# Kernel tuning notes

Measured on AMD Instinct MI355X. Metric: run time of the kernel, lower is better.

## Reference

```python
import jax, jax.numpy as jnp
import numpy as np

ITERATIONS = 10
EPS = 1e-8
ALPHA = 1.0
BETA = 1.0


def _conv3x3x3(x):
    # all-ones 3x3x3 kernel, padding=1 (SAME), single channel; NCDHW layout
    k = jnp.ones((1, 1, 3, 3, 3), x.dtype)
    return jax.lax.conv_general_dilated(
        x, k, window_strides=(1, 1, 1), padding='SAME',
        dimension_numbers=('NCDHW', 'OIDHW', 'NCDHW'))


def _soft_skeletonize(x):
    x = jax.nn.sigmoid(x)
    skeleton = x
    for _ in range(ITERATIONS):
        eroded = (_conv3x3x3(skeleton) > 0).astype(x.dtype)
        opened = (_conv3x3x3(eroded) > 0).astype(x.dtype)
        skeleton = jnp.clip(skeleton - opened, 0.0, 1.0)
    return skeleton


def _count_components(binary):
    neighbors = _conv3x3x3(binary)
    mask = binary > 0
    cnt = jnp.sum(mask).astype(binary.dtype)
    # torch.mean(neighbors[mask] + eps) == sum((neighbors+eps)*mask)/cnt
    mean_nb = jnp.sum(jnp.where(mask, neighbors + EPS, 0.0)) / jnp.maximum(cnt, 1.0)
    return (cnt / mean_nb)[None]


def setup_inputs() -> dict:
    key = jax.random.key(0)
    k1, k2 = jax.random.split(key)
    pred = jax.random.normal(k1, (2, 1, 192, 192, 192), dtype=jnp.float32)
    target = jax.random.uniform(k2, (2, 1, 192, 192, 192), dtype=jnp.float32)
    return {"pred": pred, "target": target}


def reference(pred, target):
    pred_prob = jax.nn.sigmoid(pred)
    # NOTE: module applies sigmoid again inside _soft_skeletonize (faithful)
    pred_skeleton = _soft_skeletonize(pred_prob)
    target_skeleton = _soft_skeletonize(target)

    intersection = jnp.sum(pred_skeleton * target_skeleton)
    union = jnp.sum(pred_skeleton) + jnp.sum(target_skeleton)
    skeleton_loss = 1.0 - (2.0 * intersection + EPS) / (union + EPS)

    pred_binary = (pred_prob > 0.5).astype(pred.dtype)
    target_binary = target  # .float() no-op
    pred_components = _count_components(pred_binary)
    target_components = _count_components(target_binary)
    connectivity_loss = jnp.mean(jnp.abs(pred_components - target_components))

    return ALPHA * skeleton_loss + BETA * connectivity_loss
```

## Files before the change

### kernel.cpp

```cpp
#include <hip/hip_runtime.h>
#include <math.h>

#define NN 192
#define PLANE (NN * NN)
#define VOLSZ (NN * NN * NN)
#define ZC 24
#define SLABR 8
#define NSLAB (NN / SLABR)
#define SLOTF (10 * NN)
#define NBIN 8
#define EPSF 1e-8f

template <int MODE>
__device__ __forceinline__ float bval(float u) {
  return (MODE == 0) ? ((u > 0.f) ? 1.f : 0.f) : u;
}

struct PlaneR {
  float4 a, b, c, d;
};

template <int MODE>
__device__ __forceinline__ void consume2(const PlaneR& P, float mA, float mD, float mz,
                                         int lane, float4& sY, float4& sZ,
                                         float4& cY, float4& cZ) {
  const float a0 = bval<MODE>(P.a.x), a1 = bval<MODE>(P.a.y), a2 = bval<MODE>(P.a.z), a3 = bval<MODE>(P.a.w);
  const float b0 = bval<MODE>(P.b.x), b1 = bval<MODE>(P.b.y), b2 = bval<MODE>(P.b.z), b3 = bval<MODE>(P.b.w);
  const float c0 = bval<MODE>(P.c.x), c1 = bval<MODE>(P.c.y), c2 = bval<MODE>(P.c.z), c3 = bval<MODE>(P.c.w);
  const float d0 = bval<MODE>(P.d.x), d1 = bval<MODE>(P.d.y), d2 = bval<MODE>(P.d.z), d3 = bval<MODE>(P.d.w);
  const float u0 = b0 + c0, u1 = b1 + c1, u2 = b2 + c2, u3 = b3 + c3;
  const float tY0 = fmaf(a0, mA, u0), tY1 = fmaf(a1, mA, u1), tY2 = fmaf(a2, mA, u2), tY3 = fmaf(a3, mA, u3);
  const float tZ0 = fmaf(d0, mD, u0), tZ1 = fmaf(d1, mD, u1), tZ2 = fmaf(d2, mD, u2), tZ3 = fmaf(d3, mD, u3);
  const float upY = __shfl_up(tY3, 1), dnY = __shfl_down(tY0, 1);
  const float upZ = __shfl_up(tZ3, 1), dnZ = __shfl_down(tZ0, 1);
  const float tlY = (lane == 0) ? 0.f : upY;
  const float trY = (lane >= 47) ? 0.f : dnY;
  const float tlZ = (lane == 0) ? 0.f : upZ;
  const float trZ = (lane >= 47) ? 0.f : dnZ;
  const float pY01 = tY0 + tY1, pY23 = tY2 + tY3;
  const float pZ01 = tZ0 + tZ1, pZ23 = tZ2 + tZ3;
  sY.x = (tlY + pY01) * mz; sY.y = (pY01 + tY2) * mz; sY.z = (tY1 + pY23) * mz; sY.w = (pY23 + trY) * mz;
  sZ.x = (tlZ + pZ01) * mz; sZ.y = (pZ01 + tZ2) * mz; sZ.z = (tZ1 + pZ23) * mz; sZ.w = (pZ23 + trZ) * mz;
  cY.x = b0; cY.y = b1; cY.z = b2; cY.w = b3;
  cZ.x = c0; cZ.y = c1; cZ.z = c2; cZ.w = c3;
}

#define ACC1(C, SP, SC, SN)                                   \
  {                                                           \
    float m = ((C) > 0.f) ? act : 0.f;                        \
    cnt += m;                                                 \
    acc = fmaf(m, ((SP) + (SC)) + (SN), acc);                 \
  }

#define ACCUM8(snY, snZ)                      \
  ACC1(cY.x, spY.x, scY.x, (snY).x)           \
  ACC1(cY.y, spY.y, scY.y, (snY).y)           \
  ACC1(cY.z, spY.z, scY.z, (snY).z)           \
  ACC1(cY.w, spY.w, scY.w, (snY).w)           \
  ACC1(cZ.x, spZ.x, scZ.x, (snZ).x)           \
  ACC1(cZ.y, spZ.y, scZ.y, (snZ).y)           \
  ACC1(cZ.z, spZ.z, scZ.z, (snZ).z)           \
  ACC1(cZ.w, spZ.w, scZ.w, (snZ).w)

__device__ __forceinline__ void ldsReadP(const float* pl, int slotF, int rbaseF, int xoff, PlaneR& P) {
  const float* p = pl + slotF + rbaseF;
  P.a = *(const float4*)(p + 0 * NN + xoff);
  P.b = *(const float4*)(p + 1 * NN + xoff);
  P.c = *(const float4*)(p + 2 * NN + xoff);
  P.d = *(const float4*)(p + 3 * NN + xoff);
}

__device__ __forceinline__ void stageIssue(const float* __restrict__ base, int z, int gRow0,
                                           int tid, int nQ, float4& g0, float4& g1) {
  const int zz = min(max(z, 0), NN - 1);
  const float* gp = base + (size_t)zz * PLANE + gRow0 * NN;
  g0 = *(const float4*)(gp + 4 * tid);
  if (tid + 256 < nQ) g1 = *(const float4*)(gp + 4 * (tid + 256));
}

__device__ __forceinline__ void stageWrite(float* pl, int slotF, int shiftF, int tid, int nQ,
                                           const float4& g0, const float4& g1) {
  float* q = pl + slotF + shiftF;
  *(float4*)(q + 4 * tid) = g0;
  if (tid + 256 < nQ) *(float4*)(q + 4 * (tid + 256)) = g1;
}

#define STEPX(RS, WS, DO_A, DO_B, ZLD, G0, G1, MZ)                         \
  {                                                                        \
    __syncthreads();                                                       \
    if (DO_A) stageWrite(pl, (WS) * SLOTF, shiftF, tid, nQ, G0, G1);       \
    if (DO_B) stageIssue(base, (ZLD), gRow0, tid, nQ, G0, G1);             \
    PlaneR P;                                                              \
    ldsReadP(pl, (RS) * SLOTF, rbaseF, xoff, P);                           \
    float4 snY, snZ, cnY, cnZ;                                             \
    consume2<MODE>(P, mA, mD, (MZ), lane, snY, snZ, cnY, cnZ);             \
    ACCUM8(snY, snZ);                                                      \
    spY = scY; scY = snY; spZ = scZ; scZ = snZ; cY = cnY; cZ = cnZ;        \
  }

template <int MODE>
__device__ __forceinline__ void sweep(const float* __restrict__ base, int y0, int z0,
                                      float* pl, int tid, float& cnt, float& acc) {
  const int lane = tid & 63;
  const int w = tid >> 6;
  const int xoff = 4 * min(lane, 47);
  const float act = (lane < 48) ? 1.f : 0.f;

  const bool loEdge = (y0 == 0), hiEdge = (y0 + SLABR == NN);
  const int gRow0 = loEdge ? 0 : y0 - 1;
  const int nR = 10 - (loEdge ? 1 : 0) - (hiEdge ? 1 : 0);
  const int nQ = nR * 48;
  const int shiftF = loEdge ? NN : 0;

  const int rbaseF = (2 * w) * NN;
  const float mA = (y0 + 2 * w > 0) ? 1.f : 0.f;
  const float mD = (y0 + 2 * w + 2 < NN) ? 1.f : 0.f;
  const float mzLo = (z0 > 0) ? 1.f : 0.f;
  const float mzHi = (z0 + ZC < NN) ? 1.f : 0.f;

  if (loEdge && tid < 48) {
    const float4 z4 = make_float4(0.f, 0.f, 0.f, 0.f);
#pragma unroll
    for (int r = 0; r < 4; ++r) *(float4*)(pl + r * SLOTF + 4 * tid) = z4;
  }
  if (hiEdge && tid < 48) {
    const float4 z4 = make_float4(0.f, 0.f, 0.f, 0.f);
#pragma unroll
    for (int r = 0; r < 4; ++r) *(float4*)(pl + r * SLOTF + 9 * NN + 4 * tid) = z4;
  }

  float4 a0, a1, b0, b1, c0, c1, gP0, gP1, gQ0, gQ1;
  stageIssue(base, z0 - 1, gRow0, tid, nQ, a0, a1);
  stageIssue(base, z0,     gRow0, tid, nQ, b0, b1);
  stageIssue(base, z0 + 1, gRow0, tid, nQ, c0, c1);
  stageIssue(base, z0 + 2, gRow0, tid, nQ, gP0, gP1);
  stageIssue(base, z0 + 3, gRow0, tid, nQ, gQ0, gQ1);
  stageWrite(pl, 0 * SLOTF, shiftF, tid, nQ, a0, a1);
  stageWrite(pl, 1 * SLOTF, shiftF, tid, nQ, b0, b1);
  stageWrite(pl, 2 * SLOTF, shiftF, tid, nQ, c0, c1);
  __syncthreads();

  float4 spY, scY, spZ, scZ, cY, cZ;
  {
    PlaneR P; float4 j1, j2;
    ldsReadP(pl, 0, rbaseF, xoff, P);
    consume2<MODE>(P, mA, mD, mzLo, lane, spY, spZ, j1, j2);
    ldsReadP(pl, SLOTF, rbaseF, xoff, P);
    consume2<MODE>(P, mA, mD, 1.f, lane, scY, scZ, cY, cZ);
  }

#pragma unroll 1
  for (int j = 0; j < 20; j += 4) {
    STEPX(2, 3, true, true, z0 + 4 + j + 0, gP0, gP1, 1.f);
    STEPX(3, 0, true, true, z0 + 4 + j + 1, gQ0, gQ1, 1.f);
    STEPX(0, 1, true, true, z0 + 4 + j + 2, gP0, gP1, 1.f);
    STEPX(1, 2, true, true, z0 + 4 + j + 3, gQ0, gQ1, 1.f);
  }
  STEPX(2, 3, true, true,  z0 + 24, gP0, gP1, 1.f);
  STEPX(3, 0, true, false, 0,       gQ0, gQ1, 1.f);
  STEPX(0, 1, true, false, 0,       gP0, gP1, 1.f);
  STEPX(1, 2, false, false, 0,      gQ0, gQ1, mzHi);
}

__global__ void init_ws(float* __restrict__ ws) {
  if (threadIdx.x < NBIN * 16) ws[threadIdx.x] = 0.f;
}

__global__ __launch_bounds__(256, 1) void skel_main(const float* __restrict__ pred,
                                                    const float* __restrict__ target,
                                                    float* __restrict__ ws) {
  __shared__ float pl[4 * SLOTF];
  const int b = blockIdx.x;
  const int xcd = b & 7;
  const int s = b >> 3;
  const int vol = s / NSLAB;
  const int slab = s % NSLAB;
  const int z0 = xcd * ZC;
  const int y0 = slab * SLABR;
  const float* base = (vol < 2 ? pred : target) + (size_t)(vol & 1) * VOLSZ;
  const int tid = threadIdx.x;

  float cnt = 0.f, acc = 0.f;
  if (vol < 2) sweep<0>(base, y0, z0, pl, tid, cnt, acc);
  else         sweep<1>(base, y0, z0, pl, tid, cnt, acc);

#pragma unroll
  for (int o = 32; o > 0; o >>= 1) {
    cnt += __shfl_down(cnt, o);
    acc += __shfl_down(acc, o);
  }
  __syncthreads();
  if ((tid & 63) == 0) { pl[tid >> 6] = cnt; pl[4 + (tid >> 6)] = acc; }
  __syncthreads();
  if (tid == 0) {
    const int off = (vol < 2) ? 0 : 2;
    float* sp = &ws[((slab & (NBIN - 1)) << 4) + off];
    atomicAdd(sp + 0, pl[0] + pl[1] + pl[2] + pl[3]);
    atomicAdd(sp + 1, pl[4] + pl[5] + pl[6] + pl[7]);
  }
}

__global__ void finalize(const float* __restrict__ ws, float* __restrict__ out) {
  if (threadIdx.x == 0 && blockIdx.x == 0) {
    float cp = 0.f, ap = 0.f, ct = 0.f, at = 0.f;
#pragma unroll
    for (int i = 0; i < NBIN; ++i) {
      cp += ws[i * 16 + 0];
      ap += ws[i * 16 + 1];
      ct += ws[i * 16 + 2];
      at += ws[i * 16 + 3];
    }
    float mp = (ap + EPSF * cp) / fmaxf(cp, 1.f);
    float Pc = cp / mp;
    float mt = (at + EPSF * ct) / fmaxf(ct, 1.f);
    float Tc = ct / mt;
    out[0] = fabsf(Pc - Tc);
  }
}

extern "C" void kernel_launch(void* const* d_in, const int* in_sizes, int n_in,
                              void* d_out, int out_size, void* d_ws, size_t ws_size,
                              hipStream_t stream) {
  const float* pred = (const float*)d_in[0];
  const float* target = (const float*)d_in[1];
  float* ws = (float*)d_ws;
  float* out = (float*)d_out;

  init_ws<<<1, 128, 0, stream>>>(ws);
  skel_main<<<dim3(768), dim3(256), 0, stream>>>(pred, target, ws);
  finalize<<<1, 64, 0, stream>>>(ws, out);
}
```

Measured before the change: 133.9 us.

## Halve z-chunk depth, double grid, shrink LDS ring to three slots, lighter barrier

Each block now sweeps 12 z-planes instead of 24, so the grid doubles to 1536 blocks, and the z0 mapping still keeps both halves of a z range on the same XCD. The LDS plane ring drops from four slots to three and the step loop is fully unrolled. __syncthreads is replaced by an explicit lgkmcnt wait plus s_barrier with sched barriers, so the barrier does not wait on outstanding global loads. The aim is more parallelism and occupancy; in exchange the z-halo loads are amortized over fewer planes, and the three-slot ring relies on the barrier ordering to avoid overwriting a plane still being read.

Measured after the change: 162.5 us. +21.3%, slower.

```diff
diff --git a/kernel.cpp b/kernel.cpp
--- a/kernel.cpp
+++ b/kernel.cpp
@@ -4,10 +4,11 @@
 #define NN 192
 #define PLANE (NN * NN)
 #define VOLSZ (NN * NN * NN)
-#define ZC 24
+#define ZC 12
 #define SLABR 8
 #define NSLAB (NN / SLABR)
 #define SLOTF (10 * NN)
+#define NSLOT 3
 #define NBIN 8
 #define EPSF 1e-8f
 
@@ -15,6 +16,12 @@
 __device__ __forceinline__ float bval(float u) {
   return (MODE == 0) ? ((u > 0.f) ? 1.f : 0.f) : u;
 }
+
+#define WGB()                                            \
+  asm volatile("s_waitcnt lgkmcnt(0)" ::: "memory");     \
+  __builtin_amdgcn_sched_barrier(0);                     \
+  __builtin_amdgcn_s_barrier();                          \
+  __builtin_amdgcn_sched_barrier(0);
 
 struct PlaneR {
   float4 a, b, c, d;
@@ -87,7 +94,7 @@
 
 #define STEPX(RS, WS, DO_A, DO_B, ZLD, G0, G1, MZ)                         \
   {                                                                        \
-    __syncthreads();                                                       \
+    WGB();                                                                 \
     if (DO_A) stageWrite(pl, (WS) * SLOTF, shiftF, tid, nQ, G0, G1);       \
     if (DO_B) stageIssue(base, (ZLD), gRow0, tid, nQ, G0, G1);             \
     PlaneR P;                                                              \
@@ -121,12 +128,12 @@
   if (loEdge && tid < 48) {
     const float4 z4 = make_float4(0.f, 0.f, 0.f, 0.f);
 #pragma unroll
-    for (int r = 0; r < 4; ++r) *(float4*)(pl + r * SLOTF + 4 * tid) = z4;
+    for (int r = 0; r < NSLOT; ++r) *(float4*)(pl + r * SLOTF + 4 * tid) = z4;
   }
   if (hiEdge && tid < 48) {
     const float4 z4 = make_float4(0.f, 0.f, 0.f, 0.f);
 #pragma unroll
-    for (int r = 0; r < 4; ++r) *(float4*)(pl + r * SLOTF + 9 * NN + 4 * tid) = z4;
+    for (int r = 0; r < NSLOT; ++r) *(float4*)(pl + r * SLOTF + 9 * NN + 4 * tid) = z4;
   }
 
   float4 a0, a1, b0, b1, c0, c1, gP0, gP1, gQ0, gQ1;
@@ -143,23 +150,24 @@
   float4 spY, scY, spZ, scZ, cY, cZ;
   {
     PlaneR P; float4 j1, j2;
-    ldsReadP(pl, 0, rbaseF, xoff, P);
+    ldsReadP(pl, 0 * SLOTF, rbaseF, xoff, P);
     consume2<MODE>(P, mA, mD, mzLo, lane, spY, spZ, j1, j2);
-    ldsReadP(pl, SLOTF, rbaseF, xoff, P);
+    ldsReadP(pl, 1 * SLOTF, rbaseF, xoff, P);
     consume2<MODE>(P, mA, mD, 1.f, lane, scY, scZ, cY, cZ);
   }
 
-#pragma unroll 1
-  for (int j = 0; j < 20; j += 4) {
-    STEPX(2, 3, true, true, z0 + 4 + j + 0, gP0, gP1, 1.f);
-    STEPX(3, 0, true, true, z0 + 4 + j + 1, gQ0, gQ1, 1.f);
-    STEPX(0, 1, true, true, z0 + 4 + j + 2, gP0, gP1, 1.f);
-    STEPX(1, 2, true, true, z0 + 4 + j + 3, gQ0, gQ1, 1.f);
-  }
-  STEPX(2, 3, true, true,  z0 + 24, gP0, gP1, 1.f);
-  STEPX(3, 0, true, false, 0,       gQ0, gQ1, 1.f);
+  STEPX(2, 0, true, true,  z0 + 4,  gP0, gP1, 1.f);
+  STEPX(0, 1, true, true,  z0 + 5,  gQ0, gQ1, 1.f);
+  STEPX(1, 2, true, true,  z0 + 6,  gP0, gP1, 1.f);
+  STEPX(2, 0, true, true,  z0 + 7,  gQ0, gQ1, 1.f);
+  STEPX(0, 1, true, true,  z0 + 8,  gP0, gP1, 1.f);
+  STEPX(1, 2, true, true,  z0 + 9,  gQ0, gQ1, 1.f);
+  STEPX(2, 0, true, true,  z0 + 10, gP0, gP1, 1.f);
+  STEPX(0, 1, true, true,  z0 + 11, gQ0, gQ1, 1.f);
+  STEPX(1, 2, true, true,  z0 + 12, gP0, gP1, 1.f);
+  STEPX(2, 0, true, false, 0,       gQ0, gQ1, 1.f);
   STEPX(0, 1, true, false, 0,       gP0, gP1, 1.f);
-  STEPX(1, 2, false, false, 0,      gQ0, gQ1, mzHi);
+  STEPX(1, 0, false, false, 0,      gQ0, gQ1, mzHi);
 }
 
 __global__ void init_ws(float* __restrict__ ws) {
@@ -169,13 +177,15 @@
 __global__ __launch_bounds__(256, 1) void skel_main(const float* __restrict__ pred,
                                                     const float* __restrict__ target,
                                                     float* __restrict__ ws) {
-  __shared__ float pl[4 * SLOTF];
+  __shared__ float pl[NSLOT * SLOTF];
   const int b = blockIdx.x;
   const int xcd = b & 7;
   const int s = b >> 3;
-  const int vol = s / NSLAB;
-  const int slab = s % NSLAB;
-  const int z0 = xcd * ZC;
+  const int half = s / 96;
+  const int r = s % 96;
+  const int vol = r / NSLAB;
+  const int slab = r % NSLAB;
+  const int z0 = (2 * xcd + half) * ZC;
   const int y0 = slab * SLABR;
   const float* base = (vol < 2 ? pred : target) + (size_t)(vol & 1) * VOLSZ;
   const int tid = threadIdx.x;
@@ -227,6 +237,6 @@
   float* out = (float*)d_out;
 
   init_ws<<<1, 128, 0, stream>>>(ws);
-  skel_main<<<dim3(768), dim3(256), 0, stream>>>(pred, target, ws);
+  skel_main<<<dim3(1536), dim3(256), 0, stream>>>(pred, target, ws);
   finalize<<<1, 64, 0, stream>>>(ws, out);
 }
```

## Stream z-planes directly into LDS with async global_load_lds pipelining

Applied to the files above, without the earlier changes.

Replaces the register-staged global loads and LDS stores with direct global-to-LDS loads (global_load_lds, 16 bytes per lane). Loads are issued two planes ahead and completion is tracked with explicit s_waitcnt vmcnt counts and raw s_barrier calls. The goal is to drop staging registers and the VGPR-to-LDS store instructions and to overlap loads with compute more deeply. In exchange it depends on hand-counted vmcnt values and a per-wave lane mapping, which makes the ordering fragile.

Result: no change. 133.1 us (-0.6%).

```diff
diff --git a/kernel.cpp b/kernel.cpp
--- a/kernel.cpp
+++ b/kernel.cpp
@@ -15,6 +15,11 @@
 __device__ __forceinline__ float bval(float u) {
   return (MODE == 0) ? ((u > 0.f) ? 1.f : 0.f) : u;
 }
+
+#define GLOAD16(G, L)                                                       \
+  __builtin_amdgcn_global_load_lds(                                         \
+      (const __attribute__((address_space(1))) void*)(G),                   \
+      (__attribute__((address_space(3))) void*)(L), 16, 0, 0)
 
 struct PlaneR {
   float4 a, b, c, d;
@@ -70,32 +75,30 @@
   P.d = *(const float4*)(p + 3 * NN + xoff);
 }
 
-__device__ __forceinline__ void stageIssue(const float* __restrict__ base, int z, int gRow0,
-                                           int tid, int nQ, float4& g0, float4& g1) {
+__device__ __forceinline__ void issuePlane(const float* __restrict__ base, int z,
+                                           int gRow0, float* slotBase, int lane,
+                                           int g0F, int g1F, int l0F, int l1F,
+                                           int v1e) {
   const int zz = min(max(z, 0), NN - 1);
   const float* gp = base + (size_t)zz * PLANE + gRow0 * NN;
-  g0 = *(const float4*)(gp + 4 * tid);
-  if (tid + 256 < nQ) g1 = *(const float4*)(gp + 4 * (tid + 256));
-}
-
-__device__ __forceinline__ void stageWrite(float* pl, int slotF, int shiftF, int tid, int nQ,
-                                           const float4& g0, const float4& g1) {
-  float* q = pl + slotF + shiftF;
-  *(float4*)(q + 4 * tid) = g0;
-  if (tid + 256 < nQ) *(float4*)(q + 4 * (tid + 256)) = g1;
-}
-
-#define STEPX(RS, WS, DO_A, DO_B, ZLD, G0, G1, MZ)                         \
-  {                                                                        \
-    __syncthreads();                                                       \
-    if (DO_A) stageWrite(pl, (WS) * SLOTF, shiftF, tid, nQ, G0, G1);       \
-    if (DO_B) stageIssue(base, (ZLD), gRow0, tid, nQ, G0, G1);             \
-    PlaneR P;                                                              \
-    ldsReadP(pl, (RS) * SLOTF, rbaseF, xoff, P);                           \
-    float4 snY, snZ, cnY, cnZ;                                             \
-    consume2<MODE>(P, mA, mD, (MZ), lane, snY, snZ, cnY, cnZ);             \
-    ACCUM8(snY, snZ);                                                      \
-    spY = scY; scY = snY; spZ = scZ; scZ = snZ; cY = cnY; cZ = cnZ;        \
+  GLOAD16(gp + g0F, slotBase + l0F);
+  if (lane < v1e) GLOAD16(gp + g1F, slotBase + l1F);
+}
+
+#define STEPD(RS, WS, DOI, ZLD, MZ, VMASM)                                  \
+  {                                                                         \
+    asm volatile(VMASM);                                                    \
+    __builtin_amdgcn_sched_barrier(0);                                      \
+    __builtin_amdgcn_s_barrier();                                           \
+    __builtin_amdgcn_sched_barrier(0);                                      \
+    if (DOI) issuePlane(base, (ZLD), gRow0, pl + (WS) * SLOTF + shiftF,     \
+                        lane, g0F, g1F, l0F, l1F, v1e);                     \
+    PlaneR P;                                                               \
+    ldsReadP(pl, (RS) * SLOTF, rbaseF, xoff, P);                            \
+    float4 snY, snZ, cnY, cnZ;                                              \
+    consume2<MODE>(P, mA, mD, (MZ), lane, snY, snZ, cnY, cnZ);              \
+    ACCUM8(snY, snZ);                                                       \
+    spY = scY; scY = snY; spZ = scZ; scZ = snZ; cY = cnY; cZ = cnZ;         \
   }
 
 template <int MODE>
@@ -112,6 +115,15 @@
   const int nQ = nR * 48;
   const int shiftF = loEdge ? NN : 0;
 
+  const int c1 = 4 + w;
+  const int v1 = nQ - 64 * c1;
+  const int c1e = (v1 > 0) ? c1 : 0;
+  const int v1e = (v1 > 0) ? (v1 < 64 ? v1 : 64) : 64;
+  const int l0F = 256 * w;
+  const int l1F = 256 * c1e;
+  const int g0F = 4 * (64 * w + lane);
+  const int g1F = 4 * (64 * c1e + lane);
+
   const int rbaseF = (2 * w) * NN;
   const float mA = (y0 + 2 * w > 0) ? 1.f : 0.f;
   const float mD = (y0 + 2 * w + 2 < NN) ? 1.f : 0.f;
@@ -129,37 +141,47 @@
     for (int r = 0; r < 4; ++r) *(float4*)(pl + r * SLOTF + 9 * NN + 4 * tid) = z4;
   }
 
-  float4 a0, a1, b0, b1, c0, c1, gP0, gP1, gQ0, gQ1;
-  stageIssue(base, z0 - 1, gRow0, tid, nQ, a0, a1);
-  stageIssue(base, z0,     gRow0, tid, nQ, b0, b1);
-  stageIssue(base, z0 + 1, gRow0, tid, nQ, c0, c1);
-  stageIssue(base, z0 + 2, gRow0, tid, nQ, gP0, gP1);
-  stageIssue(base, z0 + 3, gRow0, tid, nQ, gQ0, gQ1);
-  stageWrite(pl, 0 * SLOTF, shiftF, tid, nQ, a0, a1);
-  stageWrite(pl, 1 * SLOTF, shiftF, tid, nQ, b0, b1);
-  stageWrite(pl, 2 * SLOTF, shiftF, tid, nQ, c0, c1);
+  issuePlane(base, z0 - 1, gRow0, pl + 0 * SLOTF + shiftF, lane, g0F, g1F, l0F, l1F, v1e);
+  issuePlane(base, z0,     gRow0, pl + 1 * SLOTF + shiftF, lane, g0F, g1F, l0F, l1F, v1e);
+  issuePlane(base, z0 + 1, gRow0, pl + 2 * SLOTF + shiftF, lane, g0F, g1F, l0F, l1F, v1e);
+  issuePlane(base, z0 + 2, gRow0, pl + 3 * SLOTF + shiftF, lane, g0F, g1F, l0F, l1F, v1e);
   __syncthreads();
 
   float4 spY, scY, spZ, scZ, cY, cZ;
   {
     PlaneR P; float4 j1, j2;
-    ldsReadP(pl, 0, rbaseF, xoff, P);
+    ldsReadP(pl, 0 * SLOTF, rbaseF, xoff, P);
     consume2<MODE>(P, mA, mD, mzLo, lane, spY, spZ, j1, j2);
-    ldsReadP(pl, SLOTF, rbaseF, xoff, P);
+    ldsReadP(pl, 1 * SLOTF, rbaseF, xoff, P);
     consume2<MODE>(P, mA, mD, 1.f, lane, scY, scZ, cY, cZ);
   }
 
+  {
+    asm volatile("s_waitcnt vmcnt(4)");
+    __builtin_amdgcn_sched_barrier(0);
+    __builtin_amdgcn_s_barrier();
+    __builtin_amdgcn_sched_barrier(0);
+    issuePlane(base, z0 + 3, gRow0, pl + 0 * SLOTF + shiftF, lane, g0F, g1F, l0F, l1F, v1e);
+    issuePlane(base, z0 + 4, gRow0, pl + 1 * SLOTF + shiftF, lane, g0F, g1F, l0F, l1F, v1e);
+    PlaneR P;
+    ldsReadP(pl, 2 * SLOTF, rbaseF, xoff, P);
+    float4 snY, snZ, cnY, cnZ;
+    consume2<MODE>(P, mA, mD, 1.f, lane, snY, snZ, cnY, cnZ);
+    ACCUM8(snY, snZ);
+    spY = scY; scY = snY; spZ = scZ; scZ = snZ; cY = cnY; cZ = cnZ;
+  }
+
 #pragma unroll 1
-  for (int j = 0; j < 20; j += 4) {
-    STEPX(2, 3, true, true, z0 + 4 + j + 0, gP0, gP1, 1.f);
-    STEPX(3, 0, true, true, z0 + 4 + j + 1, gQ0, gQ1, 1.f);
-    STEPX(0, 1, true, true, z0 + 4 + j + 2, gP0, gP1, 1.f);
-    STEPX(1, 2, true, true, z0 + 4 + j + 3, gQ0, gQ1, 1.f);
-  }
-  STEPX(2, 3, true, true,  z0 + 24, gP0, gP1, 1.f);
-  STEPX(3, 0, true, false, 0,       gQ0, gQ1, 1.f);
-  STEPX(0, 1, true, false, 0,       gP0, gP1, 1.f);
-  STEPX(1, 2, false, false, 0,      gQ0, gQ1, mzHi);
+  for (int k = 0; k < 5; ++k) {
+    const int zb = z0 + 4 * k;
+    STEPD(3, 2, true, zb + 5, 1.f, "s_waitcnt vmcnt(4)");
+    STEPD(0, 3, true, zb + 6, 1.f, "s_waitcnt vmcnt(4)");
+    STEPD(1, 0, true, zb + 7, 1.f, "s_waitcnt vmcnt(4)");
+    STEPD(2, 1, true, zb + 8, 1.f, "s_waitcnt vmcnt(4)");
+  }
+  STEPD(3, 0, false, 0, 1.f,  "s_waitcnt vmcnt(4)");
+  STEPD(0, 0, false, 0, 1.f,  "s_waitcnt vmcnt(2)");
+  STEPD(1, 0, false, 0, mzHi, "s_waitcnt vmcnt(0)");
 }
 
 __global__ void init_ws(float* __restrict__ ws) {
```
